# Kernel optimization log

Measured on AMD Instinct MI355X. Metric: run time of the kernel, lower is better.

## Reference

```python
import jax, jax.numpy as jnp
import numpy as np

B, C, T_IN, R, TB = 8192, 3, 2048, 64, 128
ALPHA = 10.0  # steepness of sigmoid surrogate spike
Q_INIT = 6.0


def surrogate_spike(x):
    # Differentiable surrogate for the spiking nonlinearity (sigmoid fast-spike).
    return jax.nn.sigmoid(ALPHA * x)


def setup_inputs() -> dict:
    key = jax.random.key(0)
    k0, k1 = jax.random.split(key)
    traces = jax.random.normal(k0, (B, C, T_IN), jnp.float32)
    drive_w = jax.random.normal(k1, (R, C), jnp.float32) / np.sqrt(C)
    drive_b = jnp.zeros((R,), jnp.float32)
    frequency_raw = jnp.linspace(-1.2, 1.2, R, dtype=jnp.float32)
    q_center = float(np.log(np.exp(max(Q_INIT - 1.5, 1e-3)) - 1.0))  # inverse softplus
    q_raw = jnp.full((R,), q_center, jnp.float32)
    threshold_raw = jnp.zeros((R,), jnp.float32)
    return dict(traces=traces, drive_w=drive_w, drive_b=drive_b,
                frequency_raw=frequency_raw, q_raw=q_raw, threshold_raw=threshold_raw)


def reference(traces, drive_w, drive_b, frequency_raw, q_raw, threshold_raw):
    b, c, t = traces.shape
    win = t // TB  # adaptive_avg_pool1d with evenly-dividing window
    pooled = traces.reshape(b, c, TB, win).mean(axis=-1)  # [B, C, TB]
    # _normalize_traces: divide by per-sample max-abs clamped to >= 1
    scale = jnp.maximum(jnp.max(jnp.abs(pooled), axis=(1, 2), keepdims=True), 1.0)
    pooled = pooled / scale
    # 1x1 Conv1d == per-timestep linear projection C -> R
    drive = jnp.einsum('bct,rc->brt', pooled, drive_w) + drive_b[None, :, None]  # [B, R, TB]

    frequency = 0.03 + 0.17 * jax.nn.sigmoid(frequency_raw)      # [R]
    q_factor = 1.5 + jax.nn.softplus(q_raw)                      # [R]
    decay = jnp.exp(-1.0 / q_factor)                             # [R]
    threshold = 0.35 + 0.75 * jax.nn.sigmoid(threshold_raw)      # [R]

    def step(carry, current):
        state, velocity = carry
        velocity = decay * velocity + current - frequency * state
        state = state + frequency * velocity
        spikes = surrogate_spike(state - threshold)
        state = state - spikes * threshold
        return (state, velocity), spikes

    init = (jnp.zeros((b, R), drive.dtype), jnp.zeros((b, R), drive.dtype))
    drive_t = jnp.moveaxis(drive, -1, 0)  # [TB, B, R]
    _, spike_seq = jax.lax.scan(step, init, drive_t)  # spike_seq: [TB, B, R]
    return spike_seq.mean(axis=0)  # [B, R]
```

## Files before the change

### kernel.cpp

```cpp
#include <hip/hip_runtime.h>
#include <math.h>

constexpr int kC   = 3;
constexpr int kTIn = 2048;
constexpr int kR   = 64;
constexpr int kTB  = 128;
constexpr float kAlpha = 10.0f;
constexpr float kLog2e = 1.44269504088896f;

#ifndef __has_builtin
#define __has_builtin(x) 0
#endif

static __device__ __forceinline__ float fast_rcp(float x) {
#if __has_builtin(__builtin_amdgcn_rcpf)
    return __builtin_amdgcn_rcpf(x);
#else
    return 1.0f / x;
#endif
}

static __device__ __forceinline__ float fast_exp2(float x) {
#if __has_builtin(__builtin_amdgcn_exp2f)
    return __builtin_amdgcn_exp2f(x);
#else
    return __builtin_exp2f(x);
#endif
}

__global__ void param_kernel(const float* __restrict__ freq_raw,
                             const float* __restrict__ q_raw,
                             const float* __restrict__ thr_raw,
                             float* __restrict__ pp)
{
    const int r = threadIdx.x;
    if (r >= kR) return;
    const float freq  = 0.03f + 0.17f / (1.0f + expf(-freq_raw[r]));
    const float qf    = 1.5f + log1pf(expf(q_raw[r]));
    const float decay = expf(-1.0f / qf);
    const float thr   = 0.35f + 0.75f / (1.0f + expf(-thr_raw[r]));
    pp[0 * kR + r] = freq;
    pp[1 * kR + r] = decay;
    pp[2 * kR + r] = thr;
    pp[3 * kR + r] = thr * (kAlpha * kLog2e);
}

__global__ __launch_bounds__(256, 8)
void fused_encoder_kernel(const float* __restrict__ traces,
                          const float* __restrict__ drive_w,
                          const float* __restrict__ drive_b,
                          const float* __restrict__ pp,
                          float* __restrict__ out)
{
    __shared__ float sp[kTB * 4];
    __shared__ float red[4];

    const int tid  = threadIdx.x;
    const int wave = tid >> 6;
    const int lane = tid & 63;
    const long long b = blockIdx.x;

    const float4* tr4 = reinterpret_cast<const float4*>(traces)
                        + b * (kC * kTIn / 4);

    float win[6];
    #pragma unroll
    for (int j = 0; j < 6; ++j) {
        float4 v = tr4[j * 256 + tid];
        float s = (v.x + v.y) + (v.z + v.w);
        s += __shfl_xor(s, 1, 64);
        s += __shfl_xor(s, 2, 64);
        win[j] = s;
    }

    if ((tid & 3) == 0) {
        const int wq = tid >> 2;
        #pragma unroll
        for (int j = 0; j < 6; ++j) {
            int w = j * 64 + wq;
            sp[(w & 127) * 4 + (w >> 7)] = win[j];
        }
    }

    float m = 0.0f;
    #pragma unroll
    for (int j = 0; j < 6; ++j) m = fmaxf(m, fabsf(win[j]));
    #pragma unroll
    for (int off = 32; off >= 1; off >>= 1)
        m = fmaxf(m, __shfl_xor(m, off, 64));
    if (lane == 0) red[wave] = m;
    __syncthreads();

    if (wave != 0) return;

    const float summax = fmaxf(fmaxf(red[0], red[1]), fmaxf(red[2], red[3]));
    const float inv = fast_rcp(fmaxf(summax * (1.0f / 16.0f), 1.0f)) * (1.0f / 16.0f);

    const int r = lane;
    const float w0   = drive_w[r * kC + 0] * inv;
    const float w1   = drive_w[r * kC + 1] * inv;
    const float w2   = drive_w[r * kC + 2] * inv;
    const float bias = drive_b[r];
    const float freq  = pp[0 * kR + r];
    const float decay = pp[1 * kR + r];
    const float thr   = pp[2 * kR + r];
    const float thrE  = pp[3 * kR + r];
    const float expScale = kAlpha * kLog2e;

    const float4* pt = reinterpret_cast<const float4*>(sp);
    float state = 0.0f, vel = 0.0f, acc = 0.0f;
    #pragma unroll 8
    for (int t = 0; t < kTB; ++t) {
        float4 p = pt[t];
        float cur = fmaf(p.x, w0, bias);
        cur = fmaf(p.y, w1, cur);
        cur = fmaf(p.z, w2, cur);
        vel = fmaf(decay, vel, cur);
        vel = fmaf(-freq, state, vel);
        state = fmaf(freq, vel, state);
        float e = fast_exp2(fmaf(-expScale, state, thrE));
        float spike = fast_rcp(1.0f + e);
        state = fmaf(-spike, thr, state);
        acc += spike;
    }

    out[b * kR + r] = acc * (1.0f / kTB);
}

extern "C" void kernel_launch(void* const* d_in, const int* in_sizes, int n_in,
                              void* d_out, int out_size, void* d_ws, size_t ws_size,
                              hipStream_t stream)
{
    const float* traces   = (const float*)d_in[0];
    const float* drive_w  = (const float*)d_in[1];
    const float* drive_b  = (const float*)d_in[2];
    const float* freq_raw = (const float*)d_in[3];
    const float* q_raw    = (const float*)d_in[4];
    const float* thr_raw  = (const float*)d_in[5];
    float* out = (float*)d_out;
    float* pp  = (float*)d_ws;

    const int totalB = in_sizes[0] / (kC * kTIn);

    param_kernel<<<1, 64, 0, stream>>>(freq_raw, q_raw, thr_raw, pp);
    fused_encoder_kernel<<<totalB, 256, 0, stream>>>(traces, drive_w, drive_b, pp, out);
}
```

Measured before the change: 49.01 us.

## Give each wave its own samples and prefetch the next sample during the scan

Each wavefront now pools, normalizes and scans a whole sample by itself. Previously three of the four waves in a block exited after pooling while wave 0 ran the serial recurrence. Each wave loops over K samples and issues the global loads for the next sample into registers before running the current 128-step scan, so memory latency overlaps with the serial compute. The grid shrinks by a factor of 16 and each thread holds 24 float4 registers, lowering occupancy (launch bounds changed to 2). If totalB is not divisible by 16, some samples are silently skipped.

New measurement: 56.57 us. 1.15x slower.

```diff
diff --git a/kernel.cpp b/kernel.cpp
--- a/kernel.cpp
+++ b/kernel.cpp
@@ -7,6 +7,9 @@
 constexpr int kTB  = 128;
 constexpr float kAlpha = 10.0f;
 constexpr float kLog2e = 1.44269504088896f;
+
+constexpr int kK     = 4;
+constexpr int kLoads = kC * kTIn / 4 / 64;
 
 #ifndef __has_builtin
 #define __has_builtin(x) 0
@@ -28,6 +31,12 @@
 #endif
 }
 
+static __device__ __forceinline__ void sched_fence() {
+#if __has_builtin(__builtin_amdgcn_sched_barrier)
+    __builtin_amdgcn_sched_barrier(0);
+#endif
+}
+
 __global__ void param_kernel(const float* __restrict__ freq_raw,
                              const float* __restrict__ q_raw,
                              const float* __restrict__ thr_raw,
@@ -45,61 +54,25 @@
     pp[3 * kR + r] = thr * (kAlpha * kLog2e);
 }
 
-__global__ __launch_bounds__(256, 8)
+__global__ __launch_bounds__(256, 2)
 void fused_encoder_kernel(const float* __restrict__ traces,
                           const float* __restrict__ drive_w,
                           const float* __restrict__ drive_b,
                           const float* __restrict__ pp,
-                          float* __restrict__ out)
+                          float* __restrict__ out,
+                          int W, int K)
 {
-    __shared__ float sp[kTB * 4];
-    __shared__ float red[4];
-
+    __shared__ float sp_all[4][kTB * 4];
     const int tid  = threadIdx.x;
     const int wave = tid >> 6;
     const int lane = tid & 63;
-    const long long b = blockIdx.x;
-
-    const float4* tr4 = reinterpret_cast<const float4*>(traces)
-                        + b * (kC * kTIn / 4);
-
-    float win[6];
-    #pragma unroll
-    for (int j = 0; j < 6; ++j) {
-        float4 v = tr4[j * 256 + tid];
-        float s = (v.x + v.y) + (v.z + v.w);
-        s += __shfl_xor(s, 1, 64);
-        s += __shfl_xor(s, 2, 64);
-        win[j] = s;
-    }
-
-    if ((tid & 3) == 0) {
-        const int wq = tid >> 2;
-        #pragma unroll
-        for (int j = 0; j < 6; ++j) {
-            int w = j * 64 + wq;
-            sp[(w & 127) * 4 + (w >> 7)] = win[j];
-        }
-    }
-
-    float m = 0.0f;
-    #pragma unroll
-    for (int j = 0; j < 6; ++j) m = fmaxf(m, fabsf(win[j]));
-    #pragma unroll
-    for (int off = 32; off >= 1; off >>= 1)
-        m = fmaxf(m, __shfl_xor(m, off, 64));
-    if (lane == 0) red[wave] = m;
-    __syncthreads();
-
-    if (wave != 0) return;
-
-    const float summax = fmaxf(fmaxf(red[0], red[1]), fmaxf(red[2], red[3]));
-    const float inv = fast_rcp(fmaxf(summax * (1.0f / 16.0f), 1.0f)) * (1.0f / 16.0f);
+    float* sp = sp_all[wave];
+    const int gw = blockIdx.x * 4 + wave;
 
     const int r = lane;
-    const float w0   = drive_w[r * kC + 0] * inv;
-    const float w1   = drive_w[r * kC + 1] * inv;
-    const float w2   = drive_w[r * kC + 2] * inv;
+    const float w0   = drive_w[r * kC + 0];
+    const float w1   = drive_w[r * kC + 1];
+    const float w2   = drive_w[r * kC + 2];
     const float bias = drive_b[r];
     const float freq  = pp[0 * kR + r];
     const float decay = pp[1 * kR + r];
@@ -107,24 +80,64 @@
     const float thrE  = pp[3 * kR + r];
     const float expScale = kAlpha * kLog2e;
 
-    const float4* pt = reinterpret_cast<const float4*>(sp);
-    float state = 0.0f, vel = 0.0f, acc = 0.0f;
-    #pragma unroll 8
-    for (int t = 0; t < kTB; ++t) {
-        float4 p = pt[t];
-        float cur = fmaf(p.x, w0, bias);
-        cur = fmaf(p.y, w1, cur);
-        cur = fmaf(p.z, w2, cur);
-        vel = fmaf(decay, vel, cur);
-        vel = fmaf(-freq, state, vel);
-        state = fmaf(freq, vel, state);
-        float e = fast_exp2(fmaf(-expScale, state, thrE));
-        float spike = fast_rcp(1.0f + e);
-        state = fmaf(-spike, thr, state);
-        acc += spike;
+    const float4* tr4 = reinterpret_cast<const float4*>(traces);
+
+    float4 R[kLoads];
+    {
+        const float4* src = tr4 + (long long)gw * (kC * kTIn / 4) + lane;
+        #pragma unroll
+        for (int j = 0; j < kLoads; ++j) R[j] = src[j * 64];
     }
 
-    out[b * kR + r] = acc * (1.0f / kTB);
+    for (int k = 0; k < K; ++k) {
+        const long long b = (long long)k * W + gw;
+
+        float m = 0.0f;
+        #pragma unroll
+        for (int j = 0; j < kLoads; ++j) {
+            float4 v = R[j];
+            float s = (v.x + v.y) + (v.z + v.w);
+            s += __shfl_xor(s, 1, 64);
+            s += __shfl_xor(s, 2, 64);
+            m = fmaxf(m, fabsf(s));
+            if ((lane & 3) == 0) {
+                int w = j * 16 + (lane >> 2);
+                sp[(w & 127) * 4 + (w >> 7)] = s;
+            }
+        }
+        #pragma unroll
+        for (int off = 32; off >= 4; off >>= 1)
+            m = fmaxf(m, __shfl_xor(m, off, 64));
+
+        const float inv = fast_rcp(fmaxf(m * (1.0f / 16.0f), 1.0f)) * (1.0f / 16.0f);
+        const float v0 = w0 * inv, v1 = w1 * inv, v2 = w2 * inv;
+
+        if (k + 1 < K) {
+            const float4* src = tr4 + ((long long)(k + 1) * W + gw) * (kC * kTIn / 4) + lane;
+            #pragma unroll
+            for (int j = 0; j < kLoads; ++j) R[j] = src[j * 64];
+        }
+        sched_fence();
+
+        const float4* pt = reinterpret_cast<const float4*>(sp);
+        float state = 0.0f, vel = 0.0f, acc = 0.0f;
+        #pragma unroll 8
+        for (int t = 0; t < kTB; ++t) {
+            float4 p = pt[t];
+            float cur = fmaf(p.x, v0, bias);
+            cur = fmaf(p.y, v1, cur);
+            cur = fmaf(p.z, v2, cur);
+            vel = fmaf(decay, vel, cur);
+            vel = fmaf(-freq, state, vel);
+            state = fmaf(freq, vel, state);
+            float e = fast_exp2(fmaf(-expScale, state, thrE));
+            float spike = fast_rcp(1.0f + e);
+            state = fmaf(-spike, thr, state);
+            acc += spike;
+        }
+
+        out[b * kR + r] = acc * (1.0f / kTB);
+    }
 }
 
 extern "C" void kernel_launch(void* const* d_in, const int* in_sizes, int n_in,
@@ -141,7 +154,9 @@
     float* pp  = (float*)d_ws;
 
     const int totalB = in_sizes[0] / (kC * kTIn);
+    const int W = totalB / kK;
+    const int grid = W / 4;
 
     param_kernel<<<1, 64, 0, stream>>>(freq_raw, q_raw, thr_raw, pp);
-    fused_encoder_kernel<<<totalB, 256, 0, stream>>>(traces, drive_w, drive_b, pp, out);
+    fused_encoder_kernel<<<grid, 256, 0, stream>>>(traces, drive_w, drive_b, pp, out, W, kK);
 }
```

## Warp-specialize blocks: three waves pool ahead while one wave runs scan

Applied to the files above, without the earlier changes.

Each block now processes four samples. Three waves pool traces into a double-buffered shared array while a dedicated scan wave, rotated by block index and given raised priority, runs the recurrence on the previously pooled sample. This is meant to overlap global loads and pooling with the serial scan, instead of leaving three waves idle during the scan. The cost is fewer blocks (a quarter as many) and per-sample barriers. The change also assumes the batch size divides evenly by four.

Result: faster. 44.35 us (-9.5%).

```diff
diff --git a/kernel.cpp b/kernel.cpp
--- a/kernel.cpp
+++ b/kernel.cpp
@@ -7,6 +7,9 @@
 constexpr int kTB  = 128;
 constexpr float kAlpha = 10.0f;
 constexpr float kLog2e = 1.44269504088896f;
+
+constexpr int kK   = 4;
+constexpr int kF4  = kC * kTIn / 4;
 
 #ifndef __has_builtin
 #define __has_builtin(x) 0
@@ -52,79 +55,88 @@
                           const float* __restrict__ pp,
                           float* __restrict__ out)
 {
-    __shared__ float sp[kTB * 4];
-    __shared__ float red[4];
+    __shared__ float sp[2][kTB * 4];
+    __shared__ float red[2][3];
 
     const int tid  = threadIdx.x;
     const int wave = tid >> 6;
     const int lane = tid & 63;
-    const long long b = blockIdx.x;
+    const int scanWave = blockIdx.x & 3;
+    const long long base = (long long)blockIdx.x * kK;
+    const float4* tr4 = reinterpret_cast<const float4*>(traces);
 
-    const float4* tr4 = reinterpret_cast<const float4*>(traces)
-                        + b * (kC * kTIn / 4);
+    if (wave != scanWave) {
+        const int h = wave - (wave > scanWave ? 1 : 0);
 
-    float win[6];
-    #pragma unroll
-    for (int j = 0; j < 6; ++j) {
-        float4 v = tr4[j * 256 + tid];
-        float s = (v.x + v.y) + (v.z + v.w);
-        s += __shfl_xor(s, 1, 64);
-        s += __shfl_xor(s, 2, 64);
-        win[j] = s;
-    }
+        auto pool = [&](long long b, int buf) {
+            const float4* src = tr4 + b * kF4 + (h * 8) * 64 + lane;
+            float mloc = 0.0f;
+            #pragma unroll
+            for (int j = 0; j < 8; ++j) {
+                float4 v = src[j * 64];
+                float s = (v.x + v.y) + (v.z + v.w);
+                s += __shfl_xor(s, 1, 64);
+                s += __shfl_xor(s, 2, 64);
+                mloc = fmaxf(mloc, fabsf(s));
+                if ((lane & 3) == 0) {
+                    int w = (h * 8 + j) * 16 + (lane >> 2);
+                    sp[buf][(w & 127) * 4 + (w >> 7)] = s;
+                }
+            }
+            #pragma unroll
+            for (int off = 4; off <= 32; off <<= 1)
+                mloc = fmaxf(mloc, __shfl_xor(mloc, off, 64));
+            if (lane == 0) red[buf][h] = mloc;
+        };
 
-    if ((tid & 3) == 0) {
-        const int wq = tid >> 2;
-        #pragma unroll
-        for (int j = 0; j < 6; ++j) {
-            int w = j * 64 + wq;
-            sp[(w & 127) * 4 + (w >> 7)] = win[j];
+        pool(base, 0);
+        __syncthreads();
+        for (int k = 0; k < kK; ++k) {
+            if (k + 1 < kK) pool(base + k + 1, (k + 1) & 1);
+            __syncthreads();
+        }
+    } else {
+        const int r = lane;
+        const float w0   = drive_w[r * kC + 0];
+        const float w1   = drive_w[r * kC + 1];
+        const float w2   = drive_w[r * kC + 2];
+        const float bias = drive_b[r];
+        const float freq  = pp[0 * kR + r];
+        const float decay = pp[1 * kR + r];
+        const float thr   = pp[2 * kR + r];
+        const float thrE  = pp[3 * kR + r];
+        const float expScale = kAlpha * kLog2e;
+
+        __syncthreads();
+        for (int k = 0; k < kK; ++k) {
+            const int cur = k & 1;
+            const float mm = fmaxf(fmaxf(red[cur][0], red[cur][1]), red[cur][2]);
+            const float inv = fast_rcp(fmaxf(mm * (1.0f / 16.0f), 1.0f)) * (1.0f / 16.0f);
+            const float v0 = w0 * inv, v1 = w1 * inv, v2 = w2 * inv;
+            const float4* pt = reinterpret_cast<const float4*>(sp[cur]);
+
+            __builtin_amdgcn_s_setprio(1);
+            float state = 0.0f, vel = 0.0f, acc = 0.0f;
+            #pragma unroll 8
+            for (int t = 0; t < kTB; ++t) {
+                float4 p = pt[t];
+                float cur_ = fmaf(p.x, v0, bias);
+                cur_ = fmaf(p.y, v1, cur_);
+                cur_ = fmaf(p.z, v2, cur_);
+                vel = fmaf(decay, vel, cur_);
+                vel = fmaf(-freq, state, vel);
+                state = fmaf(freq, vel, state);
+                float e = fast_exp2(fmaf(-expScale, state, thrE));
+                float spike = fast_rcp(1.0f + e);
+                state = fmaf(-spike, thr, state);
+                acc += spike;
+            }
+            __builtin_amdgcn_s_setprio(0);
+
+            out[(base + k) * kR + r] = acc * (1.0f / kTB);
+            __syncthreads();
         }
     }
-
-    float m = 0.0f;
-    #pragma unroll
-    for (int j = 0; j < 6; ++j) m = fmaxf(m, fabsf(win[j]));
-    #pragma unroll
-    for (int off = 32; off >= 1; off >>= 1)
-        m = fmaxf(m, __shfl_xor(m, off, 64));
-    if (lane == 0) red[wave] = m;
-    __syncthreads();
-
-    if (wave != 0) return;
-
-    const float summax = fmaxf(fmaxf(red[0], red[1]), fmaxf(red[2], red[3]));
-    const float inv = fast_rcp(fmaxf(summax * (1.0f / 16.0f), 1.0f)) * (1.0f / 16.0f);
-
-    const int r = lane;
-    const float w0   = drive_w[r * kC + 0] * inv;
-    const float w1   = drive_w[r * kC + 1] * inv;
-    const float w2   = drive_w[r * kC + 2] * inv;
-    const float bias = drive_b[r];
-    const float freq  = pp[0 * kR + r];
-    const float decay = pp[1 * kR + r];
-    const float thr   = pp[2 * kR + r];
-    const float thrE  = pp[3 * kR + r];
-    const float expScale = kAlpha * kLog2e;
-
-    const float4* pt = reinterpret_cast<const float4*>(sp);
-    float state = 0.0f, vel = 0.0f, acc = 0.0f;
-    #pragma unroll 8
-    for (int t = 0; t < kTB; ++t) {
-        float4 p = pt[t];
-        float cur = fmaf(p.x, w0, bias);
-        cur = fmaf(p.y, w1, cur);
-        cur = fmaf(p.z, w2, cur);
-        vel = fmaf(decay, vel, cur);
-        vel = fmaf(-freq, state, vel);
-        state = fmaf(freq, vel, state);
-        float e = fast_exp2(fmaf(-expScale, state, thrE));
-        float spike = fast_rcp(1.0f + e);
-        state = fmaf(-spike, thr, state);
-        acc += spike;
-    }
-
-    out[b * kR + r] = acc * (1.0f / kTB);
 }
 
 extern "C" void kernel_launch(void* const* d_in, const int* in_sizes, int n_in,
@@ -141,7 +153,8 @@
     float* pp  = (float*)d_ws;
 
     const int totalB = in_sizes[0] / (kC * kTIn);
+    const int grid = totalB / kK;
 
     param_kernel<<<1, 64, 0, stream>>>(freq_raw, q_raw, thr_raw, pp);
-    fused_encoder_kernel<<<totalB, 256, 0, stream>>>(traces, drive_w, drive_b, pp, out);
+    fused_encoder_kernel<<<grid, 256, 0, stream>>>(traces, drive_w, drive_b, pp, out);
 }
```
